# Performance work log

Measured on AMD Instinct MI355X. Metric: run time of the kernel, lower is better.

Reference implementation:

```python
import jax, jax.numpy as jnp
import numpy as np

B, N, C, H = 2, 2048, 1024, 16
D = C // H          # head_dim = 64
HALF = D // 2       # 32 complex pairs per head


def setup_inputs() -> dict:
    key = jax.random.key(0)
    k1, k2, k3, k4 = jax.random.split(key, 4)
    x = jax.random.normal(k1, (B, N, C), dtype=jnp.float32)
    # 0.02 init scale keeps softmax logits in a sane range
    qkv_w = jax.random.normal(k2, (3 * C, C), dtype=jnp.float32) * 0.02
    proj_w = jax.random.normal(k3, (C, C), dtype=jnp.float32) * 0.02
    proj_b = jax.random.normal(k4, (C,), dtype=jnp.float32) * 0.02
    # standard RoPE frequencies: theta = 10000^{-2i/D}
    inv_freq = 1.0 / (10000.0 ** (jnp.arange(0, D, 2, dtype=jnp.float32) / D))
    angles = jnp.arange(N, dtype=jnp.float32)[:, None] * inv_freq[None, :]  # [N, HALF]
    return {
        "x": x, "qkv_w": qkv_w, "proj_w": proj_w, "proj_b": proj_b,
        "freqs_cos": jnp.cos(angles), "freqs_sin": jnp.sin(angles),
    }


def _rope(t, cos, sin):
    # t: [B, N, H, D]; cos/sin: [N, HALF] -> broadcast as [1, N, 1, HALF]
    tr = t.reshape(B, N, H, HALF, 2)
    t_re, t_im = tr[..., 0], tr[..., 1]
    c = cos[None, :, None, :]
    s = sin[None, :, None, :]
    o_re = t_re * c - t_im * s
    o_im = t_re * s + t_im * c
    return jnp.stack([o_re, o_im], axis=-1).reshape(B, N, H, D)


def reference(x, qkv_w, proj_w, proj_b, freqs_cos, freqs_sin):
    scale = D ** -0.5
    qkv = x @ qkv_w.T                              # [B, N, 3C] (no bias: qkv_bias=False)
    qkv = qkv.reshape(B, N, 3, H, D)
    q, k, v = qkv[:, :, 0], qkv[:, :, 1], qkv[:, :, 2]  # [B, N, H, D]
    q = _rope(q, freqs_cos, freqs_sin)
    k = _rope(k, freqs_cos, freqs_sin)
    scores = jnp.einsum("bqhd,bkhd->bhqk", q, k) * scale
    attn = jax.nn.softmax(scores, axis=-1)         # dropout p=0.0 -> identity
    out = jnp.einsum("bhqk,bkhd->bqhd", attn, v).reshape(B, N, C)
    return out @ proj_w.T + proj_b
```

## Files before the change

### kernel.cpp

```cpp
#include <hip/hip_runtime.h>
#include <hip/hip_bf16.h>

#define B_ 2
#define N_ 2048
#define C_ 1024
#define H_ 16
#define D_ 64
#define HALF_ 32

typedef __attribute__((ext_vector_type(8))) __bf16 bf16x8;
typedef __attribute__((ext_vector_type(8))) unsigned short u16x8;
typedef __attribute__((ext_vector_type(4))) float f32x4;
typedef __attribute__((ext_vector_type(16))) float f32x16;

__device__ __forceinline__ unsigned short f2bf(float f) {
  union { float f; unsigned u; } v; v.f = f;
  unsigned r = v.u + 0x7FFFu + ((v.u >> 16) & 1u);
  return (unsigned short)(r >> 16);
}

__device__ __forceinline__ unsigned cvt_pk_bf16(float lo, float hi) {
  unsigned r;
  asm("v_cvt_pk_bf16_f32 %0, %1, %2" : "=v"(r) : "v"(lo), "v"(hi));
  return r;
}

__device__ __forceinline__ void gload_lds16(const void* g, void* l) {
  __builtin_amdgcn_global_load_lds(
      (const __attribute__((address_space(1))) void*)g,
      (__attribute__((address_space(3))) void*)l, 16, 0, 0);
}

__global__ __launch_bounds__(256) void cast3_f32_bf16(
    const float* __restrict__ a, const float* __restrict__ b,
    const float* __restrict__ c, unsigned short* __restrict__ oa,
    unsigned short* __restrict__ ob, unsigned short* __restrict__ oc) {
  int i = blockIdx.x * 256 + threadIdx.x;
  const float4* src;
  ushort4* dst;
  int off;
  if (i < 1048576) {
    src = (const float4*)a; dst = (ushort4*)oa; off = i;
  } else if (i < 1835008) {
    src = (const float4*)b; dst = (ushort4*)ob; off = i - 1048576;
  } else {
    src = (const float4*)c; dst = (ushort4*)oc; off = i - 1835008;
  }
  float4 v = src[off];
  ushort4 o;
  o.x = f2bf(v.x); o.y = f2bf(v.y); o.z = f2bf(v.z); o.w = f2bf(v.w);
  dst[off] = o;
}

template <int EPI>
__global__ __launch_bounds__(256) void gemm_bt(
    const unsigned short* __restrict__ A, const unsigned short* __restrict__ Bw,
    int M, int Nn, int K,
    float* __restrict__ Cout, const float* __restrict__ bias,
    unsigned short* __restrict__ qo, unsigned short* __restrict__ ko,
    unsigned short* __restrict__ vto,
    const float* __restrict__ cosT, const float* __restrict__ sinT) {
  __shared__ __align__(16) unsigned short As[128][64];
  __shared__ __align__(16) unsigned short Bs[128][64];
  const int tid = threadIdx.x;
  const int lane = tid & 63;
  const int wid = tid >> 6;
  const int wm = wid >> 1, wn = wid & 1;
  const int l15 = lane & 15;
  const int g = lane >> 4;
  const int m0 = blockIdx.x * 128;
  const int n0 = blockIdx.y * 128;

  const int srow = wid * 8 + (lane >> 3);
  const int scol = (lane & 7) * 8;

  f32x4 acc[4][4] = {};

  const int nK = K >> 6;
  for (int kt = 0; kt < nK; ++kt) {
    __syncthreads();
#pragma unroll
    for (int j = 0; j < 4; ++j) {
      gload_lds16(&A[(size_t)(m0 + j * 32 + srow) * K + kt * 64 + scol],
                  &As[j * 32 + wid * 8][0]);
      gload_lds16(&Bw[(size_t)(n0 + j * 32 + srow) * K + kt * 64 + scol],
                  &Bs[j * 32 + wid * 8][0]);
    }
    __syncthreads();
#pragma unroll
    for (int kk = 0; kk < 2; ++kk) {
      bf16x8 af[4], bfv[4];
#pragma unroll
      for (int m = 0; m < 4; ++m)
        af[m] = *reinterpret_cast<const bf16x8*>(&As[wm * 64 + m * 16 + l15][kk * 32 + g * 8]);
#pragma unroll
      for (int n = 0; n < 4; ++n)
        bfv[n] = *reinterpret_cast<const bf16x8*>(&Bs[wn * 64 + n * 16 + l15][kk * 32 + g * 8]);
#pragma unroll
      for (int m = 0; m < 4; ++m)
#pragma unroll
        for (int n = 0; n < 4; ++n)
          acc[m][n] = __builtin_amdgcn_mfma_f32_16x16x32_bf16(af[m], bfv[n], acc[m][n], 0, 0, 0);
    }
  }

  if constexpr (EPI == 0) {
#pragma unroll
    for (int n = 0; n < 4; ++n) {
      int col = n0 + wn * 64 + n * 16 + l15;
      float bv = bias[col];
#pragma unroll
      for (int m = 0; m < 4; ++m) {
        int rbase = m0 + wm * 64 + m * 16 + g * 4;
#pragma unroll
        for (int r = 0; r < 4; ++r)
          Cout[(size_t)(rbase + r) * Nn + col] = acc[m][n][r] + bv;
      }
    }
  } else {
    const int which = n0 >> 10;
    if (which == 2) {
#pragma unroll
      for (int m = 0; m < 4; ++m)
#pragma unroll
        for (int n = 0; n < 4; ++n) {
          int col = n0 + wn * 64 + n * 16 + l15;
          int hc = col & 1023;
          int hh = hc >> 6, d = hc & 63;
          int row0 = m0 + wm * 64 + m * 16 + g * 4;
          int seq0 = row0 & (N_ - 1), bb = row0 >> 11;
          int seqP = (seq0 & ~12) | ((seq0 & 4) << 1) | ((seq0 & 8) >> 1);
          ushort4 pk;
          pk.x = f2bf(acc[m][n][0]); pk.y = f2bf(acc[m][n][1]);
          pk.z = f2bf(acc[m][n][2]); pk.w = f2bf(acc[m][n][3]);
          *reinterpret_cast<ushort4*>(
              &vto[(((size_t)bb * H_ + hh) * D_ + d) * N_ + seqP]) = pk;
        }
    } else {
      unsigned short* dst = (which == 0) ? qo : ko;
      const float qscale = (which == 0) ? 0.125f * 1.44269504f : 1.0f;
#pragma unroll
      for (int m = 0; m < 4; ++m)
#pragma unroll
        for (int n = 0; n < 4; ++n)
#pragma unroll
          for (int r = 0; r < 4; ++r) {
            int col = n0 + wn * 64 + n * 16 + l15;
            int row = m0 + wm * 64 + m * 16 + g * 4 + r;
            float val = acc[m][n][r];
            float partner = __shfl_xor(val, 1);
            int hc = col & 1023;
            int hh = hc >> 6, d = hc & 63;
            int seq = row & (N_ - 1), bb = row >> 11;
            float cs = cosT[seq * HALF_ + (d >> 1)];
            float sn = sinT[seq * HALF_ + (d >> 1)];
            float res = (d & 1) ? (partner * sn + val * cs) : (val * cs - partner * sn);
            res *= qscale;
            dst[(((size_t)bb * H_ + hh) * N_ + seq) * D_ + d] = f2bf(res);
          }
    }
  }
}

__global__ __launch_bounds__(512) void attn_kernel(
    const unsigned short* __restrict__ q,
    const unsigned short* __restrict__ k,
    const unsigned short* __restrict__ vt,
    unsigned short* __restrict__ o) {
  __shared__ __align__(16) unsigned short Kl[2][64][64];
  __shared__ __align__(16) unsigned short Vl[2][64][64];

  const int tid = threadIdx.x;
  const int lane = tid & 63;
  const int w = tid >> 6;
  const int l31 = lane & 31;
  const int hi = lane >> 5;

  const int bid = blockIdx.x;
  const int nat = (bid & 7) * 32 + (bid >> 3);
  const int qt = nat & 7;
  const int bh = nat >> 3;
  const int b = bh >> 4, h = bh & 15;

  const size_t hk = (size_t)bh * N_ * D_;
  const size_t hv = (size_t)bh * D_ * N_;
  const int qrow = qt * 256 + w * 32 + l31;

  bf16x8 qf[4];
#pragma unroll
  for (int kt = 0; kt < 4; ++kt)
    qf[kt] = *reinterpret_cast<const bf16x8*>(
        &q[hk + (size_t)qrow * D_ + kt * 16 + hi * 8]);

  const int prow = tid >> 3;
  const int pchk = tid & 7;
  const int swz = (pchk ^ (prow & 7)) * 8;

  u16x8 kr, vr;
  auto issue = [&](int t) {
    kr = *reinterpret_cast<const u16x8*>(&k[hk + (size_t)(t * 64 + prow) * D_ + pchk * 8]);
    vr = *reinterpret_cast<const u16x8*>(&vt[hv + (size_t)prow * N_ + t * 64 + pchk * 8]);
  };
  auto commit = [&](int buf) {
    *reinterpret_cast<u16x8*>(&Kl[buf][prow][swz]) = kr;
    *reinterpret_cast<u16x8*>(&Vl[buf][prow][swz]) = vr;
  };

  issue(0);
  commit(0);
  __syncthreads();

  f32x16 accO[2] = {};
  float lrun = 0.f;
  const int b7 = l31 & 7;

  const int NT = N_ / 64;
  for (int t = 0; t < NT; ++t) {
    const int cur = t & 1;
    if (t + 1 < NT) issue(t + 1);

    f32x16 s[2] = {};
    __builtin_amdgcn_s_setprio(1);
#pragma unroll
    for (int kb = 0; kb < 2; ++kb)
#pragma unroll
      for (int kt = 0; kt < 4; ++kt) {
        bf16x8 kf = *reinterpret_cast<const bf16x8*>(
            &Kl[cur][kb * 32 + l31][(((kt * 2 + hi) ^ b7)) * 8]);
        s[kb] = __builtin_amdgcn_mfma_f32_32x32x16_bf16(kf, qf[kt], s[kb], 0, 0, 0);
      }
    __builtin_amdgcn_s_setprio(0);

#pragma unroll
    for (int kb = 0; kb < 2; ++kb)
#pragma unroll
      for (int i = 0; i < 16; ++i) s[kb][i] = __builtin_exp2f(s[kb][i]);

    float sloc[16];
#pragma unroll
    for (int i = 0; i < 16; ++i) sloc[i] = s[0][i] + s[1][i];
#pragma unroll
    for (int st = 8; st > 0; st >>= 1)
#pragma unroll
      for (int i = 0; i < 8; ++i)
        if (i < st) sloc[i] += sloc[i + st];
    {
      unsigned ua = __float_as_uint(sloc[0]), ub = ua;
      auto r = __builtin_amdgcn_permlane32_swap(ua, ub, false, false);
      lrun += __uint_as_float(r[0]) + __uint_as_float(r[1]);
    }

    bf16x8 PA[4];
#pragma unroll
    for (int kvc = 0; kvc < 4; ++kvc) {
      const int kb = kvc >> 1, base = (kvc & 1) * 8;
      union { unsigned u[4]; bf16x8 v; } pa;
#pragma unroll
      for (int wd = 0; wd < 4; ++wd)
        pa.u[wd] = cvt_pk_bf16(s[kb][base + 2 * wd], s[kb][base + 2 * wd + 1]);
      PA[kvc] = pa.v;
    }

    __builtin_amdgcn_s_setprio(1);
#pragma unroll
    for (int db = 0; db < 2; ++db)
#pragma unroll
      for (int kvc = 0; kvc < 4; ++kvc) {
        bf16x8 vf = *reinterpret_cast<const bf16x8*>(
            &Vl[cur][db * 32 + l31][(((kvc * 2 + hi) ^ b7)) * 8]);
        accO[db] = __builtin_amdgcn_mfma_f32_32x32x16_bf16(vf, PA[kvc], accO[db], 0, 0, 0);
      }
    __builtin_amdgcn_s_setprio(0);

    if (t + 1 < NT) commit(cur ^ 1);
    __syncthreads();
  }

  float rl = 1.0f / lrun;
  const size_t obase = ((size_t)b * N_ + qrow) * C_ + h * 64;
#pragma unroll
  for (int db = 0; db < 2; ++db)
#pragma unroll
    for (int rg = 0; rg < 4; ++rg) {
      ushort4 pk;
      pk.x = f2bf(accO[db][rg * 4 + 0] * rl);
      pk.y = f2bf(accO[db][rg * 4 + 1] * rl);
      pk.z = f2bf(accO[db][rg * 4 + 2] * rl);
      pk.w = f2bf(accO[db][rg * 4 + 3] * rl);
      *reinterpret_cast<ushort4*>(&o[obase + db * 32 + rg * 8 + hi * 4]) = pk;
    }
}

extern "C" void kernel_launch(void* const* d_in, const int* in_sizes, int n_in,
                              void* d_out, int out_size, void* d_ws, size_t ws_size,
                              hipStream_t stream) {
  const float* x      = (const float*)d_in[0];
  const float* qkv_w  = (const float*)d_in[1];
  const float* proj_w = (const float*)d_in[2];
  const float* proj_b = (const float*)d_in[3];
  const float* cosT   = (const float*)d_in[4];
  const float* sinT   = (const float*)d_in[5];
  float* out = (float*)d_out;

  unsigned short* xb     = (unsigned short*)d_ws;
  unsigned short* wqkvb  = xb + (size_t)4096 * 1024;
  unsigned short* wprojb = wqkvb + (size_t)3072 * 1024;
  unsigned short* qb     = wprojb + (size_t)1024 * 1024;
  unsigned short* kb     = qb + (size_t)32 * 2048 * 64;
  unsigned short* vtb    = kb + (size_t)32 * 2048 * 64;
  unsigned short* ab     = vtb + (size_t)32 * 2048 * 64;

  cast3_f32_bf16<<<8192, 256, 0, stream>>>(x, qkv_w, proj_w, xb, wqkvb, wprojb);

  dim3 g1(4096 / 128, 3072 / 128);
  gemm_bt<1><<<g1, 256, 0, stream>>>(xb, wqkvb, 4096, 3072, 1024,
                                     nullptr, nullptr, qb, kb, vtb, cosT, sinT);

  attn_kernel<<<256, 512, 0, stream>>>(qb, kb, vtb, ab);

  dim3 g3(4096 / 128, 1024 / 128);
  gemm_bt<0><<<g3, 256, 0, stream>>>(ab, wprojb, 4096, 1024, 1024,
                                     out, proj_b, nullptr, nullptr, nullptr,
                                     nullptr, nullptr);
}
```

Measured before the change: 144.3 us.

## Software-pipeline attention QK and PV across tiles; remap GEMM blocks XCD-aware

The attention loop is restructured so the QK^T MFMAs for tile t run alongside the softmax and PV MFMAs for tile t-1. K is prefetched one tile ahead and V is loaded for the current tile, with score registers ping-ponged between two sets. Separately, both GEMMs now use a 1D grid whose block index is remapped so consecutive blocks on the same XCD share neighbouring tiles, aiming at better L2 locality. The pipelining raises register pressure because two score tiles are live at once.

Result: slower. 147.9 us (+2.5%).

```diff
diff --git a/kernel.cpp b/kernel.cpp
--- a/kernel.cpp
+++ b/kernel.cpp
@@ -68,8 +68,13 @@
   const int wm = wid >> 1, wn = wid & 1;
   const int l15 = lane & 15;
   const int g = lane >> 4;
-  const int m0 = blockIdx.x * 128;
-  const int n0 = blockIdx.y * 128;
+
+  const int per = gridDim.x >> 3;
+  const int f = blockIdx.x;
+  const int nat = (f & 7) * per + (f >> 3);
+  const int mtiles = M >> 7;
+  const int m0 = (nat % mtiles) * 128;
+  const int n0 = (nat / mtiles) * 128;
 
   const int srow = wid * 8 + (lane >> 3);
   const int scol = (lane & 7) * 8;
@@ -197,84 +202,109 @@
   const int swz = (pchk ^ (prow & 7)) * 8;
 
   u16x8 kr, vr;
-  auto issue = [&](int t) {
+  auto issueK = [&](int t) {
     kr = *reinterpret_cast<const u16x8*>(&k[hk + (size_t)(t * 64 + prow) * D_ + pchk * 8]);
+  };
+  auto issueV = [&](int t) {
     vr = *reinterpret_cast<const u16x8*>(&vt[hv + (size_t)prow * N_ + t * 64 + pchk * 8]);
   };
-  auto commit = [&](int buf) {
-    *reinterpret_cast<u16x8*>(&Kl[buf][prow][swz]) = kr;
-    *reinterpret_cast<u16x8*>(&Vl[buf][prow][swz]) = vr;
-  };
-
-  issue(0);
-  commit(0);
-  __syncthreads();
+  auto commitK = [&](int buf) { *reinterpret_cast<u16x8*>(&Kl[buf][prow][swz]) = kr; };
+  auto commitV = [&](int buf) { *reinterpret_cast<u16x8*>(&Vl[buf][prow][swz]) = vr; };
 
   f32x16 accO[2] = {};
   float lrun = 0.f;
   const int b7 = l31 & 7;
-
   const int NT = N_ / 64;
-  for (int t = 0; t < NT; ++t) {
-    const int cur = t & 1;
-    if (t + 1 < NT) issue(t + 1);
-
-    f32x16 s[2] = {};
-    __builtin_amdgcn_s_setprio(1);
-#pragma unroll
-    for (int kb = 0; kb < 2; ++kb)
-#pragma unroll
-      for (int kt = 0; kt < 4; ++kt) {
-        bf16x8 kf = *reinterpret_cast<const bf16x8*>(
-            &Kl[cur][kb * 32 + l31][(((kt * 2 + hi) ^ b7)) * 8]);
-        s[kb] = __builtin_amdgcn_mfma_f32_32x32x16_bf16(kf, qf[kt], s[kb], 0, 0, 0);
-      }
-    __builtin_amdgcn_s_setprio(0);
-
-#pragma unroll
-    for (int kb = 0; kb < 2; ++kb)
-#pragma unroll
-      for (int i = 0; i < 16; ++i) s[kb][i] = __builtin_exp2f(s[kb][i]);
-
-    float sloc[16];
-#pragma unroll
-    for (int i = 0; i < 16; ++i) sloc[i] = s[0][i] + s[1][i];
-#pragma unroll
-    for (int st = 8; st > 0; st >>= 1)
-#pragma unroll
-      for (int i = 0; i < 8; ++i)
-        if (i < st) sloc[i] += sloc[i + st];
-    {
-      unsigned ua = __float_as_uint(sloc[0]), ub = ua;
-      auto r = __builtin_amdgcn_permlane32_swap(ua, ub, false, false);
-      lrun += __uint_as_float(r[0]) + __uint_as_float(r[1]);
-    }
-
-    bf16x8 PA[4];
-#pragma unroll
-    for (int kvc = 0; kvc < 4; ++kvc) {
-      const int kb = kvc >> 1, base = (kvc & 1) * 8;
-      union { unsigned u[4]; bf16x8 v; } pa;
-#pragma unroll
-      for (int wd = 0; wd < 4; ++wd)
-        pa.u[wd] = cvt_pk_bf16(s[kb][base + 2 * wd], s[kb][base + 2 * wd + 1]);
-      PA[kvc] = pa.v;
-    }
-
-    __builtin_amdgcn_s_setprio(1);
-#pragma unroll
-    for (int db = 0; db < 2; ++db)
-#pragma unroll
-      for (int kvc = 0; kvc < 4; ++kvc) {
-        bf16x8 vf = *reinterpret_cast<const bf16x8*>(
-            &Vl[cur][db * 32 + l31][(((kvc * 2 + hi) ^ b7)) * 8]);
-        accO[db] = __builtin_amdgcn_mfma_f32_32x32x16_bf16(vf, PA[kvc], accO[db], 0, 0, 0);
-      }
-    __builtin_amdgcn_s_setprio(0);
-
-    if (t + 1 < NT) commit(cur ^ 1);
-    __syncthreads();
+
+  f32x16 sA[2], sB[2];
+
+#define QK_MFMA(T, SC)                                                        \
+  do {                                                                        \
+    f32x16 z_ = {};                                                           \
+    SC[0] = z_; SC[1] = z_;                                                   \
+    __builtin_amdgcn_s_setprio(1);                                            \
+    _Pragma("unroll")                                                         \
+    for (int kb = 0; kb < 2; ++kb)                                            \
+      _Pragma("unroll")                                                       \
+      for (int kt = 0; kt < 4; ++kt) {                                        \
+        bf16x8 kf = *reinterpret_cast<const bf16x8*>(                         \
+            &Kl[(T) & 1][kb * 32 + l31][(((kt * 2 + hi) ^ b7)) * 8]);         \
+        SC[kb] = __builtin_amdgcn_mfma_f32_32x32x16_bf16(kf, qf[kt], SC[kb], 0, 0, 0); \
+      }                                                                       \
+    __builtin_amdgcn_s_setprio(0);                                            \
+  } while (0)
+
+#define SMPV(SP, VB)                                                          \
+  do {                                                                        \
+    _Pragma("unroll")                                                         \
+    for (int kb = 0; kb < 2; ++kb)                                            \
+      _Pragma("unroll")                                                       \
+      for (int i = 0; i < 16; ++i) SP[kb][i] = __builtin_exp2f(SP[kb][i]);    \
+    float sloc[16];                                                           \
+    _Pragma("unroll")                                                         \
+    for (int i = 0; i < 16; ++i) sloc[i] = SP[0][i] + SP[1][i];               \
+    _Pragma("unroll")                                                         \
+    for (int st = 8; st > 0; st >>= 1)                                        \
+      _Pragma("unroll")                                                       \
+      for (int i = 0; i < 8; ++i)                                             \
+        if (i < st) sloc[i] += sloc[i + st];                                  \
+    {                                                                         \
+      unsigned ua = __float_as_uint(sloc[0]), ub = ua;                        \
+      auto rr = __builtin_amdgcn_permlane32_swap(ua, ub, false, false);       \
+      lrun += __uint_as_float(rr[0]) + __uint_as_float(rr[1]);                \
+    }                                                                         \
+    bf16x8 PA[4];                                                             \
+    _Pragma("unroll")                                                         \
+    for (int kvc = 0; kvc < 4; ++kvc) {                                       \
+      const int kb = kvc >> 1, base = (kvc & 1) * 8;                          \
+      union { unsigned u[4]; bf16x8 v; } pa;                                  \
+      _Pragma("unroll")                                                       \
+      for (int wd = 0; wd < 4; ++wd)                                          \
+        pa.u[wd] = cvt_pk_bf16(SP[kb][base + 2 * wd], SP[kb][base + 2 * wd + 1]); \
+      PA[kvc] = pa.v;                                                         \
+    }                                                                         \
+    __builtin_amdgcn_s_setprio(1);                                            \
+    _Pragma("unroll")                                                         \
+    for (int db = 0; db < 2; ++db)                                            \
+      _Pragma("unroll")                                                       \
+      for (int kvc = 0; kvc < 4; ++kvc) {                                     \
+        bf16x8 vf = *reinterpret_cast<const bf16x8*>(                         \
+            &Vl[VB][db * 32 + l31][(((kvc * 2 + hi) ^ b7)) * 8]);             \
+        accO[db] = __builtin_amdgcn_mfma_f32_32x32x16_bf16(vf, PA[kvc], accO[db], 0, 0, 0); \
+      }                                                                       \
+    __builtin_amdgcn_s_setprio(0);                                            \
+  } while (0)
+
+#define BODY(T, SP, SC)                                                       \
+  do {                                                                        \
+    const int t_ = (T);                                                       \
+    if (t_ + 1 < NT) issueK(t_ + 1);                                          \
+    issueV(t_);                                                               \
+    QK_MFMA(t_, SC);                                                          \
+    SMPV(SP, (t_ - 1) & 1);                                                   \
+    if (t_ + 1 < NT) commitK((t_ + 1) & 1);                                   \
+    commitV(t_ & 1);                                                          \
+    __syncthreads();                                                          \
+  } while (0)
+
+  issueK(0);
+  commitK(0);
+  __syncthreads();
+
+  issueK(1);
+  issueV(0);
+  QK_MFMA(0, sA);
+  commitK(1);
+  commitV(0);
+  __syncthreads();
+
+  for (int tt = 1; tt + 1 < NT; tt += 2) {
+    BODY(tt, sA, sB);
+    BODY(tt + 1, sB, sA);
   }
+  BODY(NT - 1, sA, sB);
+
+  SMPV(sB, (NT - 1) & 1);
 
   float rl = 1.0f / lrun;
   const size_t obase = ((size_t)b * N_ + qrow) * C_ + h * 64;
@@ -289,6 +319,9 @@
       pk.w = f2bf(accO[db][rg * 4 + 3] * rl);
       *reinterpret_cast<ushort4*>(&o[obase + db * 32 + rg * 8 + hi * 4]) = pk;
     }
+#undef BODY
+#undef SMPV
+#undef QK_MFMA
 }
 
 extern "C" void kernel_launch(void* const* d_in, const int* in_sizes, int n_in,
@@ -312,14 +345,12 @@
 
   cast3_f32_bf16<<<8192, 256, 0, stream>>>(x, qkv_w, proj_w, xb, wqkvb, wprojb);
 
-  dim3 g1(4096 / 128, 3072 / 128);
-  gemm_bt<1><<<g1, 256, 0, stream>>>(xb, wqkvb, 4096, 3072, 1024,
-                                     nullptr, nullptr, qb, kb, vtb, cosT, sinT);
+  gemm_bt<1><<<768, 256, 0, stream>>>(xb, wqkvb, 4096, 3072, 1024,
+                                      nullptr, nullptr, qb, kb, vtb, cosT, sinT);
 
   attn_kernel<<<256, 512, 0, stream>>>(qb, kb, vtb, ab);
 
-  dim3 g3(4096 / 128, 1024 / 128);
-  gemm_bt<0><<<g3, 256, 0, stream>>>(ab, wprojb, 4096, 1024, 1024,
-                                     out, proj_b, nullptr, nullptr, nullptr,
-                                     nullptr, nullptr);
-}
+  gemm_bt<0><<<256, 256, 0, stream>>>(ab, wprojb, 4096, 1024, 1024,
+                                      out, proj_b, nullptr, nullptr, nullptr,
+                                      nullptr, nullptr);
+}
```
